# Kernel optimization log

Measured on AMD Instinct MI355X. Metric: run time of the kernel, lower is better.

The kernel has to match this reference:

```python
import jax, jax.numpy as jnp
import numpy as np

B, D, H, O, E = 8192, 1024, 4096, 1024, 3

def setup_inputs() -> dict:
    key = jax.random.key(0)
    ks = jax.random.split(key, 8)
    s = lambda fan_in: 1.0 / np.sqrt(fan_in)
    return {
        "x":   jax.random.normal(ks[0], (B, D), jnp.float32),
        "gw1": jax.random.normal(ks[1], (D, 256), jnp.float32) * s(D),
        "gb1": jnp.zeros((256,), jnp.float32),
        "gw2": jax.random.normal(ks[2], (256, 128), jnp.float32) * s(256),
        "gb2": jnp.zeros((128,), jnp.float32),
        "gw3": jax.random.normal(ks[3], (128, E), jnp.float32) * s(128),
        "gb3": jnp.zeros((E,), jnp.float32),
        "ew1": jax.random.normal(ks[4], (E, D, H), jnp.float32) * s(D),
        "eb1": jnp.zeros((E, H), jnp.float32),
        "ew2": jax.random.normal(ks[5], (E, H, O), jnp.float32) * s(H),
        "eb2": jnp.zeros((E, O), jnp.float32),
        "top_k": 2,
    }

def reference(x, gw1, gb1, gw2, gb2, gw3, gb3, ew1, eb1, ew2, eb2, top_k):
    # Gating network (dropout is identity in eval mode)
    g = jax.nn.relu(x @ gw1 + gb1)
    g = jax.nn.relu(g @ gw2 + gb2)
    gates = jax.nn.softmax(g @ gw3 + gb3, axis=-1)          # [B, E]

    # top-k routing with renormalized weights
    topk_scores, topk_idx = jax.lax.top_k(gates, top_k)     # [B, k]
    topk_scores = topk_scores / jnp.sum(topk_scores, axis=-1, keepdims=True)

    # scatter normalized scores into dense [B, E] combine weights
    b_ix = jnp.arange(x.shape[0])[:, None]
    combine = jnp.zeros_like(gates).at[b_ix, topk_idx].add(topk_scores)  # [B, E]

    # run all experts densely (small E=3), combine with routing weights
    eh = jax.nn.relu(jnp.einsum('bd,edh->beh', x, ew1) + eb1[None])      # [B, E, H]
    eo = jnp.einsum('beh,eho->beo', eh, ew2) + eb2[None]                 # [B, E, O]
    out = jnp.einsum('be,beo->bo', combine, eo)                          # [B, O]
    return out, gates
```

## Files before the change

### kernel.cpp

```cpp
#include <hip/hip_runtime.h>
#include <cstdint>
#include <cstddef>

#define B_ROWS 8192
#define D_DIM  1024
#define H_DIM  4096
#define O_DIM  1024
#define E_NUM  3
#define K2     (2 * H_DIM)
#define MT256  34
#define SLOT_MAX (MT256 * 256)

typedef __attribute__((ext_vector_type(4))) float f4;
typedef __attribute__((ext_vector_type(8))) _Float16 half8;

__device__ __forceinline__ unsigned short f2h_bits(float f) {
  _Float16 h = (_Float16)f;
  return __builtin_bit_cast(unsigned short, h);
}

__device__ __forceinline__ void async16(const void* g, void* l) {
  __builtin_amdgcn_global_load_lds(
      (const __attribute__((address_space(1))) unsigned int*)g,
      (__attribute__((address_space(3))) unsigned int*)l, 16, 0, 0);
}

__global__ __launch_bounds__(256) void k_cast_x(const float* __restrict__ in,
                                                unsigned short* __restrict__ out) {
  size_t i = (size_t)blockIdx.x * 256 + threadIdx.x;
  const f4* p = (const f4*)in;
  f4 a = p[2 * i], b = p[2 * i + 1];
  half8 h;
#pragma unroll
  for (int j = 0; j < 4; ++j) { h[j] = (_Float16)a[j]; h[4 + j] = (_Float16)b[j]; }
  *(half8*)(out + 8 * i) = h;
}

__global__ __launch_bounds__(256) void k_transpose_cast(const float* __restrict__ in,
                                                        unsigned short* __restrict__ out,
                                                        int R, int C) {
  __shared__ float tile[32][33];
  const size_t eoff = (size_t)blockIdx.z * R * C;
  const float* I = in + eoff;
  unsigned short* O = out + eoff;
  int c0 = blockIdx.x * 32, r0 = blockIdx.y * 32;
  int tx = threadIdx.x & 31, ty = threadIdx.x >> 5;
#pragma unroll
  for (int i = 0; i < 4; ++i)
    tile[ty + 8 * i][tx] = I[(size_t)(r0 + ty + 8 * i) * C + c0 + tx];
  __syncthreads();
#pragma unroll
  for (int i = 0; i < 4; ++i)
    O[(size_t)(c0 + ty + 8 * i) * R + r0 + tx] = f2h_bits(tile[tx][ty + 8 * i]);
}

__global__ __launch_bounds__(256) void k_gemm_f32(const float* __restrict__ A,
                                                  const float* __restrict__ Bm,
                                                  const float* __restrict__ bias,
                                                  float* __restrict__ C,
                                                  int N, int K) {
  __shared__ float sAT[16][68];
  __shared__ float sB[16][68];
  const int t = threadIdx.x;
  const int tx = t & 15, ty = t >> 4;
  const int m0 = blockIdx.y * 64, n0 = blockIdx.x * 64;
  float acc[4][4] = {};
  for (int k0 = 0; k0 < K; k0 += 16) {
    __syncthreads();
#pragma unroll
    for (int i = 0; i < 4; ++i) {
      int idx = t + i * 256;
      int r = idx >> 4, c = idx & 15;
      sAT[c][r] = A[(size_t)(m0 + r) * K + (k0 + c)];
      int rb = idx >> 6, cb = idx & 63;
      sB[rb][cb] = Bm[(size_t)(k0 + rb) * N + (n0 + cb)];
    }
    __syncthreads();
#pragma unroll
    for (int kk = 0; kk < 16; ++kk) {
      f4 av = *(const f4*)&sAT[kk][ty * 4];
      f4 bv = *(const f4*)&sB[kk][tx * 4];
#pragma unroll
      for (int i = 0; i < 4; ++i)
#pragma unroll
        for (int j = 0; j < 4; ++j)
          acc[i][j] = fmaf(av[i], bv[j], acc[i][j]);
    }
  }
#pragma unroll
  for (int i = 0; i < 4; ++i) {
    int row = m0 + ty * 4 + i;
    f4 v;
#pragma unroll
    for (int j = 0; j < 4; ++j)
      v[j] = fmaxf(acc[i][j] + bias[n0 + tx * 4 + j], 0.f);
    *(f4*)&C[(size_t)row * N + n0 + tx * 4] = v;
  }
}

__global__ __launch_bounds__(256) void k_gate_topk(const float* __restrict__ h2,
                                                   const float* __restrict__ gw3,
                                                   const float* __restrict__ gb3,
                                                   float* __restrict__ gates,
                                                   float* __restrict__ combine,
                                                   int* __restrict__ bucket) {
  const int lane = threadIdx.x & 63;
  const int row = blockIdx.x * 4 + (threadIdx.x >> 6);
  const float* h = h2 + (size_t)row * 128;
  float h0 = h[lane], h1 = h[lane + 64];
  float l0 = h0 * gw3[lane * 3 + 0] + h1 * gw3[(lane + 64) * 3 + 0];
  float l1 = h0 * gw3[lane * 3 + 1] + h1 * gw3[(lane + 64) * 3 + 1];
  float l2 = h0 * gw3[lane * 3 + 2] + h1 * gw3[(lane + 64) * 3 + 2];
#pragma unroll
  for (int off = 32; off > 0; off >>= 1) {
    l0 += __shfl_down(l0, off);
    l1 += __shfl_down(l1, off);
    l2 += __shfl_down(l2, off);
  }
  if (lane == 0) {
    float g0 = l0 + gb3[0], g1v = l1 + gb3[1], g2v = l2 + gb3[2];
    float mx = fmaxf(g0, fmaxf(g1v, g2v));
    float e0 = expf(g0 - mx), e1 = expf(g1v - mx), e2 = expf(g2v - mx);
    float inv = 1.f / (e0 + e1 + e2);
    float p0 = e0 * inv, p1 = e1 * inv, p2 = e2 * inv;
    gates[row * 3 + 0] = p0; gates[row * 3 + 1] = p1; gates[row * 3 + 2] = p2;
    int amin = 0; float pm = p0;
    if (p1 <= pm) { pm = p1; amin = 1; }
    if (p2 <= pm) { pm = p2; amin = 2; }
    float denom = (p0 + p1 + p2) - pm;
    combine[row * 3 + 0] = (amin == 0) ? 0.f : p0 / denom;
    combine[row * 3 + 1] = (amin == 1) ? 0.f : p1 / denom;
    combine[row * 3 + 2] = (amin == 2) ? 0.f : p2 / denom;
    bucket[row] = amin;
  }
}

__global__ __launch_bounds__(256) void k_count(const int* __restrict__ bucket,
                                               int* __restrict__ cnt) {
  int row = blockIdx.x * 256 + threadIdx.x;
  int b = bucket[row];
  int lane = threadIdx.x & 63;
#pragma unroll
  for (int bid = 0; bid < 3; ++bid) {
    unsigned long long m = __ballot(b == bid);
    if (m && b == bid) {
      int prefix = __popcll(m & ((1ull << lane) - 1));
      if (prefix == 0) atomicAdd(&cnt[bid], __popcll(m));
    }
  }
}

__global__ void k_meta(const int* __restrict__ cnt, int* __restrict__ meta,
                       int* __restrict__ cnt2) {
  int t0 = (cnt[0] + 255) >> 8;
  int t1 = (cnt[1] + 255) >> 8;
  int t2 = (cnt[2] + 255) >> 8;
  meta[0] = 0; meta[1] = t0; meta[2] = t0 + t1; meta[3] = t0 + t1 + t2;
  cnt2[0] = 0; cnt2[1] = 0; cnt2[2] = 0;
}

__global__ __launch_bounds__(256) void k_scatter(const int* __restrict__ bucket,
                                                 const int* __restrict__ meta,
                                                 int* __restrict__ cnt2,
                                                 int* __restrict__ sorted) {
  int row = blockIdx.x * 256 + threadIdx.x;
  int b = bucket[row];
  int lane = threadIdx.x & 63;
#pragma unroll
  for (int bid = 0; bid < 3; ++bid) {
    unsigned long long m = __ballot(b == bid);
    if (m) {
      int cntm = __popcll(m);
      int leader = __ffsll((unsigned long long)m) - 1;
      int base = 0;
      if (lane == leader) base = atomicAdd(&cnt2[bid], cntm);
      base = __shfl(base, leader);
      if (b == bid) {
        int prefix = __popcll(m & ((1ull << lane) - 1));
        sorted[meta[bid] * 256 + base + prefix] = row;
      }
    }
  }
}

__device__ __forceinline__ void bucket_experts(int b, int& ea, int& eb) {
  ea = (b == 0) ? 1 : 0;
  eb = (b == 2) ? 1 : 2;
}


#define BAR8()  do { __builtin_amdgcn_s_barrier(); __builtin_amdgcn_sched_barrier(0); } while (0)
#define LGKM0() do { asm volatile("s_waitcnt lgkmcnt(0)" ::: "memory"); __builtin_amdgcn_sched_barrier(0); } while (0)
#define VMW(n)  do { asm volatile("s_waitcnt vmcnt(" #n ")" ::: "memory"); __builtin_amdgcn_sched_barrier(0); } while (0)

#define STG_A(buf, h, kt) do { \
    async16(aptr[(h) * 2 + 0] + (size_t)(kt) * 64, smem + (buf) * 32768 + (h) * 16384 + t * 16); \
    async16(aptr[(h) * 2 + 1] + (size_t)(kt) * 64, smem + (buf) * 32768 + (h) * 16384 + 8192 + t * 16); \
  } while (0)
#define STG_B(buf, h, kt) do { \
    async16(bptr[(h) * 2 + 0] + (size_t)(kt) * 64, smem + 65536 + (buf) * 32768 + (h) * 16384 + t * 16); \
    async16(bptr[(h) * 2 + 1] + (size_t)(kt) * 64, smem + 65536 + (buf) * 32768 + (h) * 16384 + 8192 + t * 16); \
  } while (0)
#define LDA8(buf, mh) do { \
    _Pragma("unroll") \
    for (int mf = 0; mf < 4; ++mf) { \
      fa[mf][0] = *(const half8*)(smem + (buf) * 32768 + baseA + (mh) * 8192 + mf * 2048 + ck0); \
      fa[mf][1] = *(const half8*)(smem + (buf) * 32768 + baseA + (mh) * 8192 + mf * 2048 + ck1); \
    } } while (0)
#define LDB8(buf, nh) do { \
    _Pragma("unroll") \
    for (int nf2 = 0; nf2 < 2; ++nf2) { \
      fb[(nh) * 2 + nf2][0] = *(const half8*)(smem + (buf) * 32768 + baseB + ((nh) * 2 + nf2) * 2048 + ck0); \
      fb[(nh) * 2 + nf2][1] = *(const half8*)(smem + (buf) * 32768 + baseB + ((nh) * 2 + nf2) * 2048 + ck1); \
    } } while (0)
#define MM8(mh, nh) do { \
    _Pragma("unroll") \
    for (int mf = 0; mf < 4; ++mf) { \
      _Pragma("unroll") \
      for (int nf2 = 0; nf2 < 2; ++nf2) { \
        acc[(mh) * 4 + mf][(nh) * 2 + nf2] = __builtin_amdgcn_mfma_f32_16x16x32_f16( \
            fa[mf][0], fb[(nh) * 2 + nf2][0], acc[(mh) * 4 + mf][(nh) * 2 + nf2], 0, 0, 0); \
        acc[(mh) * 4 + mf][(nh) * 2 + nf2] = __builtin_amdgcn_mfma_f32_16x16x32_f16( \
            fa[mf][1], fb[(nh) * 2 + nf2][1], acc[(mh) * 4 + mf][(nh) * 2 + nf2], 0, 0, 0); \
      } } } while (0)

#define KLOOP8(NITER, LASTKT) \
  _Pragma("unroll 1") \
  for (int it = 0; it < (NITER) - 1; ++it) { \
    const int kt = 2 * it; \
    LDA8(0, 0); LDB8(0, 0); STG_A(1, 0, kt + 1); \
    BAR8(); LGKM0(); \
    __builtin_amdgcn_s_setprio(1); MM8(0, 0); __builtin_amdgcn_s_setprio(0); \
    BAR8(); \
    LDB8(0, 1); STG_A(1, 1, kt + 1); \
    BAR8(); LGKM0(); \
    __builtin_amdgcn_s_setprio(1); MM8(0, 1); __builtin_amdgcn_s_setprio(0); \
    BAR8(); \
    LDA8(0, 1); STG_B(0, 0, kt + 2); \
    BAR8(); LGKM0(); \
    __builtin_amdgcn_s_setprio(1); MM8(1, 0); __builtin_amdgcn_s_setprio(0); \
    BAR8(); \
    STG_A(0, 0, kt + 2); \
    BAR8(); LGKM0(); \
    __builtin_amdgcn_s_setprio(1); MM8(1, 1); __builtin_amdgcn_s_setprio(0); \
    VMW(4); BAR8(); \
    LDA8(1, 0); LDB8(1, 0); STG_A(0, 1, kt + 2); \
    BAR8(); LGKM0(); \
    __builtin_amdgcn_s_setprio(1); MM8(0, 0); __builtin_amdgcn_s_setprio(0); \
    BAR8(); \
    LDB8(1, 1); STG_B(0, 1, kt + 2); \
    BAR8(); LGKM0(); \
    __builtin_amdgcn_s_setprio(1); MM8(0, 1); __builtin_amdgcn_s_setprio(0); \
    BAR8(); \
    LDA8(1, 1); STG_B(1, 0, kt + 3); \
    BAR8(); LGKM0(); \
    __builtin_amdgcn_s_setprio(1); MM8(1, 0); __builtin_amdgcn_s_setprio(0); \
    BAR8(); \
    STG_B(1, 1, kt + 3); \
    BAR8(); LGKM0(); \
    __builtin_amdgcn_s_setprio(1); MM8(1, 1); __builtin_amdgcn_s_setprio(0); \
    VMW(4); BAR8(); \
  } \
  {  \
    LDA8(0, 0); LDB8(0, 0); STG_A(1, 0, LASTKT); \
    BAR8(); LGKM0(); \
    __builtin_amdgcn_s_setprio(1); MM8(0, 0); __builtin_amdgcn_s_setprio(0); \
    BAR8(); \
    LDB8(0, 1); STG_A(1, 1, LASTKT); \
    BAR8(); LGKM0(); \
    __builtin_amdgcn_s_setprio(1); MM8(0, 1); __builtin_amdgcn_s_setprio(0); \
    BAR8(); \
    LDA8(0, 1); \
    BAR8(); LGKM0(); \
    __builtin_amdgcn_s_setprio(1); MM8(1, 0); __builtin_amdgcn_s_setprio(0); \
    BAR8(); \
    BAR8(); LGKM0(); \
    __builtin_amdgcn_s_setprio(1); MM8(1, 1); __builtin_amdgcn_s_setprio(0); \
    VMW(0); BAR8(); \
    LDA8(1, 0); LDB8(1, 0); MM8(0, 0); \
    LDB8(1, 1); MM8(0, 1); \
    LDA8(1, 1); MM8(1, 0); \
    MM8(1, 1); \
  }

__global__ __launch_bounds__(512, 2) void k_expert_h8(const unsigned short* __restrict__ Xh,
                                                      const unsigned short* __restrict__ W1T,
                                                      const float* __restrict__ combine,
                                                      const float* __restrict__ eb1,
                                                      const int* __restrict__ sorted,
                                                      const int* __restrict__ meta,
                                                      unsigned short* __restrict__ EHS) {
  constexpr int K = D_DIM;
  const int mt = blockIdx.x;
  const int tb1 = meta[1], tb2 = meta[2], tb3 = meta[3];
  if (mt >= tb3) return;
  const int b = (mt >= tb2) ? 2 : (mt >= tb1) ? 1 : 0;
  int ea, ebx; bucket_experts(b, ea, ebx);
  const int z = blockIdx.z;
  const int e = z ? ebx : ea;
  const int slot0 = mt * 256;
  const int n0 = blockIdx.y * 256;

  __shared__ __align__(16) char smem[131072];
  __shared__ float sC[256];
  const int t = threadIdx.x;
  if (t < 256) {
    int r = sorted[slot0 + t];
    sC[t] = (r < 0) ? 0.f : combine[(size_t)r * 3 + e];
  }

  const int jrow = t >> 3;
  const int j = (t & 7) ^ (jrow & 7);
  const unsigned short* aptr[4];
  const unsigned short* bptr[4];
#pragma unroll
  for (int i = 0; i < 4; ++i) {
    int R = jrow + i * 64;
    int r = sorted[slot0 + R];
    int rr = (r < 0) ? 0 : r;
    aptr[i] = Xh + (size_t)rr * K + j * 8;
    bptr[i] = W1T + (size_t)e * H_DIM * K + (size_t)(n0 + R) * K + j * 8;
  }
  const int lane = t & 63;
  const int wid = t >> 6;
  const int wm = wid >> 2, wn = wid & 3;
  const int quad = lane >> 4, l16 = lane & 15;
  const int ck0 = ((quad) ^ (l16 & 7)) * 16;
  const int ck1 = ((4 + quad) ^ (l16 & 7)) * 16;
  const int baseA = (wm * 128 + l16) * 128;
  const int baseB = 65536 + (wn * 64 + l16) * 128;

  f4 acc[8][4] = {};
  half8 fa[4][2], fb[4][2];

  STG_A(0, 0, 0); STG_A(0, 1, 0); STG_B(0, 0, 0); STG_B(0, 1, 0);
  STG_B(1, 0, 1); STG_B(1, 1, 1);
  VMW(4); BAR8();

  KLOOP8(8, 15)

  const float* bias = eb1 + (size_t)e * H_DIM;
#pragma unroll
  for (int nf = 0; nf < 4; ++nf) {
    int col = n0 + wn * 64 + nf * 16 + l16;
    float bb = bias[col];
#pragma unroll
    for (int mf = 0; mf < 8; ++mf) {
#pragma unroll
      for (int r = 0; r < 4; ++r) {
        int rloc = wm * 128 + mf * 16 + quad * 4 + r;
        float v = fmaxf(acc[mf][nf][r] + bb, 0.f) * sC[rloc];
        EHS[(size_t)(slot0 + rloc) * K2 + (size_t)z * H_DIM + col] = f2h_bits(v);
      }
    }
  }
}

__global__ __launch_bounds__(512, 2) void k_expert_o8(const unsigned short* __restrict__ EHS,
                                                      const unsigned short* __restrict__ W2T,
                                                      const float* __restrict__ combine,
                                                      const float* __restrict__ eb2,
                                                      const int* __restrict__ sorted,
                                                      const int* __restrict__ meta,
                                                      float* __restrict__ dst,
                                                      int osplit, int use_atomic) {
  const int mt = blockIdx.x;
  const int tb1 = meta[1], tb2 = meta[2], tb3 = meta[3];
  if (mt >= tb3) return;
  const int b = (mt >= tb2) ? 2 : (mt >= tb1) ? 1 : 0;
  int ea, ebx; bucket_experts(b, ea, ebx);
  const int hz = blockIdx.z;
  const int half = osplit >> 1;
  const int e = (hz < half) ? ea : ebx;
  const int kchunk = K2 / osplit;
  const int koff_b = (hz % half) * kchunk;
  const int slot0 = mt * 256;
  const int n0 = blockIdx.y * 256;

  __shared__ __align__(16) char smem[131072];
  __shared__ int sRow[256];
  __shared__ float sCa[256], sCb[256];
  const int t = threadIdx.x;
  if (t < 256) {
    int r = sorted[slot0 + t];
    sRow[t] = r;
    int rr = (r < 0) ? 0 : r;
    sCa[t] = combine[(size_t)rr * 3 + ea];
    sCb[t] = combine[(size_t)rr * 3 + ebx];
  }

  const int jrow = t >> 3;
  const int j = (t & 7) ^ (jrow & 7);
  const unsigned short* aptr[4];
  const unsigned short* bptr[4];
#pragma unroll
  for (int i = 0; i < 4; ++i) {
    int R = jrow + i * 64;
    aptr[i] = EHS + (size_t)(slot0 + R) * K2 + (size_t)hz * kchunk + j * 8;
    bptr[i] = W2T + (size_t)e * O_DIM * H_DIM + (size_t)(n0 + R) * H_DIM + koff_b + j * 8;
  }
  const int lane = t & 63;
  const int wid = t >> 6;
  const int wm = wid >> 2, wn = wid & 3;
  const int quad = lane >> 4, l16 = lane & 15;
  const int ck0 = ((quad) ^ (l16 & 7)) * 16;
  const int ck1 = ((4 + quad) ^ (l16 & 7)) * 16;
  const int baseA = (wm * 128 + l16) * 128;
  const int baseB = 65536 + (wn * 64 + l16) * 128;

  f4 acc[8][4] = {};
  half8 fa[4][2], fb[4][2];

  STG_A(0, 0, 0); STG_A(0, 1, 0); STG_B(0, 0, 0); STG_B(0, 1, 0);
  STG_B(1, 0, 1); STG_B(1, 1, 1);
  VMW(4); BAR8();

  const int niter = kchunk / 128;
  const int lastkt = 2 * niter - 1;
  KLOOP8(niter, lastkt)

  float* part = use_atomic ? dst : dst + (size_t)hz * B_ROWS * O_DIM;
#pragma unroll
  for (int nf = 0; nf < 4; ++nf) {
    int col = n0 + wn * 64 + nf * 16 + l16;
    float ba = eb2[(size_t)ea * O_DIM + col];
    float bb = eb2[(size_t)ebx * O_DIM + col];
#pragma unroll
    for (int mf = 0; mf < 8; ++mf) {
#pragma unroll
      for (int r = 0; r < 4; ++r) {
        int rloc = wm * 128 + mf * 16 + quad * 4 + r;
        int rowg = sRow[rloc];
        if (rowg >= 0) {
          float v = acc[mf][nf][r];
          if (hz == 0) v += sCa[rloc] * ba + sCb[rloc] * bb;
          if (use_atomic) atomicAdd(&part[(size_t)rowg * O_DIM + col], v);
          else            part[(size_t)rowg * O_DIM + col] = v;
        }
      }
    }
  }
}

__global__ __launch_bounds__(256) void k_reduceN(const float* __restrict__ parts,
                                                 float* __restrict__ out, int n) {
  const size_t S = (size_t)B_ROWS * O_DIM;
  size_t i = ((size_t)blockIdx.x * 256 + threadIdx.x) * 4;
  f4 v = *(const f4*)(parts + i);
#pragma unroll 1
  for (int p = 1; p < n; ++p) v += *(const f4*)(parts + (size_t)p * S + i);
  *(f4*)(out + i) = v;
}

extern "C" void kernel_launch(void* const* d_in, const int* in_sizes, int n_in,
                              void* d_out, int out_size, void* d_ws, size_t ws_size,
                              hipStream_t stream) {
  const float* x   = (const float*)d_in[0];
  const float* gw1 = (const float*)d_in[1];
  const float* gb1 = (const float*)d_in[2];
  const float* gw2 = (const float*)d_in[3];
  const float* gb2 = (const float*)d_in[4];
  const float* gw3 = (const float*)d_in[5];
  const float* gb3 = (const float*)d_in[6];
  const float* ew1 = (const float*)d_in[7];
  const float* eb1 = (const float*)d_in[8];
  const float* ew2 = (const float*)d_in[9];
  const float* eb2 = (const float*)d_in[10];
  float* out = (float*)d_out;
  float* gates = out + (size_t)B_ROWS * O_DIM;

  char* ws = (char*)d_ws;
  size_t off = 0;
  auto take = [&](size_t bytes) -> char* {
    char* p = ws + off;
    off += (bytes + 255) & ~(size_t)255;
    return p;
  };
  unsigned short* xh  = (unsigned short*)take((size_t)B_ROWS * D_DIM * 2);
  unsigned short* w1t = (unsigned short*)take((size_t)E_NUM * H_DIM * D_DIM * 2);
  unsigned short* w2t = (unsigned short*)take((size_t)E_NUM * O_DIM * H_DIM * 2);
  float* comb   = (float*)take((size_t)B_ROWS * 3 * 4);
  float* g1     = (float*)take((size_t)B_ROWS * 256 * 4);
  float* h2     = (float*)take((size_t)B_ROWS * 128 * 4);
  int* bucket   = (int*)take((size_t)B_ROWS * 4);
  int* sorted   = (int*)take((size_t)SLOT_MAX * 4);
  int* cnt      = (int*)take(3 * 4);
  int* cnt2     = (int*)take(3 * 4);
  int* meta     = (int*)take(4 * 4);
  unsigned short* ehs = (unsigned short*)take((size_t)SLOT_MAX * K2 * 2);

  const size_t part_bytes = (size_t)B_ROWS * O_DIM * 4;
  int osplit, use_atomic;
  float* o8_dst;
  if (off + 4 * part_bytes + 1024 <= ws_size) {
    osplit = 4; use_atomic = 0;
    o8_dst = (float*)take(4 * part_bytes);
  } else if (off + 2 * part_bytes + 1024 <= ws_size) {
    osplit = 2; use_atomic = 0;
    o8_dst = (float*)take(2 * part_bytes);
  } else {
    osplit = 2; use_atomic = 1;
    o8_dst = out;
  }

  hipMemsetAsync(cnt, 0, 3 * 4, stream);
  hipMemsetAsync(sorted, 0xFF, (size_t)SLOT_MAX * 4, stream);
  if (use_atomic)
    hipMemsetAsync(out, 0, (size_t)B_ROWS * O_DIM * 4, stream);

  k_cast_x<<<dim3(B_ROWS * D_DIM / (256 * 8)), 256, 0, stream>>>(x, xh);
  k_transpose_cast<<<dim3(H_DIM / 32, D_DIM / 32, E_NUM), 256, 0, stream>>>(ew1, w1t, D_DIM, H_DIM);
  k_transpose_cast<<<dim3(O_DIM / 32, H_DIM / 32, E_NUM), 256, 0, stream>>>(ew2, w2t, H_DIM, O_DIM);

  k_gemm_f32<<<dim3(256 / 64, B_ROWS / 64), 256, 0, stream>>>(x, gw1, gb1, g1, 256, D_DIM);
  k_gemm_f32<<<dim3(128 / 64, B_ROWS / 64), 256, 0, stream>>>(g1, gw2, gb2, h2, 128, 256);
  k_gate_topk<<<dim3(B_ROWS / 4), 256, 0, stream>>>(h2, gw3, gb3, gates, comb, bucket);

  k_count<<<dim3(B_ROWS / 256), 256, 0, stream>>>(bucket, cnt);
  k_meta<<<1, 1, 0, stream>>>(cnt, meta, cnt2);
  k_scatter<<<dim3(B_ROWS / 256), 256, 0, stream>>>(bucket, meta, cnt2, sorted);

  k_expert_h8<<<dim3(MT256, H_DIM / 256, 2), 512, 0, stream>>>(
      xh, w1t, comb, eb1, sorted, meta, ehs);
  k_expert_o8<<<dim3(MT256, O_DIM / 256, osplit), 512, 0, stream>>>(
      ehs, w2t, comb, eb2, sorted, meta, o8_dst, osplit, use_atomic);
  if (!use_atomic)
    k_reduceN<<<dim3(B_ROWS * O_DIM / (256 * 4)), 256, 0, stream>>>(o8_dst, out, osplit);
}
```

Measured before the change: 751.5 us.

## Rebalance expert output GEMM with flat grid and split-K tail tiles

Replaces the 3D output-GEMM grid (M tiles × N tiles × osplit K-splits) with a flat grid. The first 256 work items run the full per-expert K, and the leftover tiles are split four ways along K and accumulated with atomics into zeroed partial buffers. A small kernel zeroes the tail regions beforehand, and the final reduction now sums only two partials instead of four. The aim is to cut the wave-quantization tail and the extra partial-buffer traffic, at the cost of atomic adds on the tail tiles and one extra launch.

```diff
diff --git a/kernel.cpp b/kernel.cpp
--- a/kernel.cpp
+++ b/kernel.cpp
@@ -10,6 +10,7 @@
 #define K2     (2 * H_DIM)
 #define MT256  34
 #define SLOT_MAX (MT256 * 256)
+#define OGRID  320
 
 typedef __attribute__((ext_vector_type(4))) float f4;
 typedef __attribute__((ext_vector_type(8))) _Float16 half8;
@@ -356,6 +357,22 @@
   }
 }
 
+__global__ __launch_bounds__(256) void k_zero_ov(const int* __restrict__ sorted,
+                                                 const int* __restrict__ meta,
+                                                 float* __restrict__ parts) {
+  const int T = meta[3] * 8;
+  const int w = 256 + blockIdx.x;
+  if (w >= T) return;
+  const int mt = w >> 3, rem = w & 7, n0i = rem >> 1, hz = rem & 1;
+  const int r = threadIdx.x;
+  int rowg = sorted[mt * 256 + r];
+  if (rowg < 0) return;
+  float* p = parts + (size_t)hz * B_ROWS * O_DIM + (size_t)rowg * O_DIM + n0i * 256;
+  f4 z = {0.f, 0.f, 0.f, 0.f};
+#pragma unroll
+  for (int c = 0; c < 256; c += 4) *(f4*)(p + c) = z;
+}
+
 __global__ __launch_bounds__(512, 2) void k_expert_o8(const unsigned short* __restrict__ EHS,
                                                       const unsigned short* __restrict__ W2T,
                                                       const float* __restrict__ combine,
@@ -363,19 +380,28 @@
                                                       const int* __restrict__ sorted,
                                                       const int* __restrict__ meta,
                                                       float* __restrict__ dst,
-                                                      int osplit, int use_atomic) {
-  const int mt = blockIdx.x;
+                                                      int use_atomic) {
   const int tb1 = meta[1], tb2 = meta[2], tb3 = meta[3];
-  if (mt >= tb3) return;
+  const int T = tb3 * 8;
+  const int bid = blockIdx.x;
+  int w, q, niter;
+  bool is_sub;
+  if (bid < 256) {
+    if (bid >= T) return;
+    w = bid; q = 0; niter = 32; is_sub = false;
+  } else {
+    int sid = bid - 256;
+    w = 256 + (sid >> 2);
+    if (w >= T) return;
+    q = sid & 3; niter = 8; is_sub = true;
+  }
+  const int mt = w >> 3, rem = w & 7;
+  const int n0 = ((rem >> 1) & 3) * 256;
+  const int hz = rem & 1;
   const int b = (mt >= tb2) ? 2 : (mt >= tb1) ? 1 : 0;
   int ea, ebx; bucket_experts(b, ea, ebx);
-  const int hz = blockIdx.z;
-  const int half = osplit >> 1;
-  const int e = (hz < half) ? ea : ebx;
-  const int kchunk = K2 / osplit;
-  const int koff_b = (hz % half) * kchunk;
+  const int e = hz ? ebx : ea;
   const int slot0 = mt * 256;
-  const int n0 = blockIdx.y * 256;
 
   __shared__ __align__(16) char smem[131072];
   __shared__ int sRow[256];
@@ -396,8 +422,8 @@
 #pragma unroll
   for (int i = 0; i < 4; ++i) {
     int R = jrow + i * 64;
-    aptr[i] = EHS + (size_t)(slot0 + R) * K2 + (size_t)hz * kchunk + j * 8;
-    bptr[i] = W2T + (size_t)e * O_DIM * H_DIM + (size_t)(n0 + R) * H_DIM + koff_b + j * 8;
+    aptr[i] = EHS + (size_t)(slot0 + R) * K2 + (size_t)hz * H_DIM + q * 1024 + j * 8;
+    bptr[i] = W2T + (size_t)e * O_DIM * H_DIM + (size_t)(n0 + R) * H_DIM + q * 1024 + j * 8;
   }
   const int lane = t & 63;
   const int wid = t >> 6;
@@ -415,11 +441,11 @@
   STG_B(1, 0, 1); STG_B(1, 1, 1);
   VMW(4); BAR8();
 
-  const int niter = kchunk / 128;
   const int lastkt = 2 * niter - 1;
   KLOOP8(niter, lastkt)
 
-  float* part = use_atomic ? dst : dst + (size_t)hz * B_ROWS * O_DIM;
+  float* base = use_atomic ? dst : dst + (size_t)hz * B_ROWS * O_DIM;
+  const bool do_store = !is_sub && !use_atomic;
 #pragma unroll
   for (int nf = 0; nf < 4; ++nf) {
     int col = n0 + wn * 64 + nf * 16 + l16;
@@ -433,9 +459,10 @@
         int rowg = sRow[rloc];
         if (rowg >= 0) {
           float v = acc[mf][nf][r];
-          if (hz == 0) v += sCa[rloc] * ba + sCb[rloc] * bb;
-          if (use_atomic) atomicAdd(&part[(size_t)rowg * O_DIM + col], v);
-          else            part[(size_t)rowg * O_DIM + col] = v;
+          if (hz == 0 && q == 0) v += sCa[rloc] * ba + sCb[rloc] * bb;
+          size_t idx = (size_t)rowg * O_DIM + col;
+          if (do_store) base[idx] = v;
+          else atomicAdd(&base[idx], v);
         }
       }
     }
@@ -490,16 +517,13 @@
   unsigned short* ehs = (unsigned short*)take((size_t)SLOT_MAX * K2 * 2);
 
   const size_t part_bytes = (size_t)B_ROWS * O_DIM * 4;
-  int osplit, use_atomic;
+  int use_atomic;
   float* o8_dst;
-  if (off + 4 * part_bytes + 1024 <= ws_size) {
-    osplit = 4; use_atomic = 0;
-    o8_dst = (float*)take(4 * part_bytes);
-  } else if (off + 2 * part_bytes + 1024 <= ws_size) {
-    osplit = 2; use_atomic = 0;
+  if (off + 2 * part_bytes + 1024 <= ws_size) {
+    use_atomic = 0;
     o8_dst = (float*)take(2 * part_bytes);
   } else {
-    osplit = 2; use_atomic = 1;
+    use_atomic = 1;
     o8_dst = out;
   }
 
@@ -522,8 +546,10 @@
 
   k_expert_h8<<<dim3(MT256, H_DIM / 256, 2), 512, 0, stream>>>(
       xh, w1t, comb, eb1, sorted, meta, ehs);
-  k_expert_o8<<<dim3(MT256, O_DIM / 256, osplit), 512, 0, stream>>>(
-      ehs, w2t, comb, eb2, sorted, meta, o8_dst, osplit, use_atomic);
   if (!use_atomic)
-    k_reduceN<<<dim3(B_ROWS * O_DIM / (256 * 4)), 256, 0, stream>>>(o8_dst, out, osplit);
-}
+    k_zero_ov<<<dim3(64), 256, 0, stream>>>(sorted, meta, o8_dst);
+  k_expert_o8<<<dim3(OGRID), 512, 0, stream>>>(
+      ehs, w2t, comb, eb2, sorted, meta, o8_dst, use_atomic);
+  if (!use_atomic)
+    k_reduceN<<<dim3(B_ROWS * O_DIM / (256 * 4)), 256, 0, stream>>>(o8_dst, out, 2);
+}
```

New measurement: 763.7 us. No clear change (+1.6%).
